# Performance work log

Measured on AMD Instinct MI355X. Metric: run time of the kernel, lower is better.

The kernel has to match this reference:

```python
import jax, jax.numpy as jnp
import numpy as np

B, S, D = 2, 2048, 4096
H, HD = 32, 128  # n_heads, head_dim
P = 30           # prefix_len
ROPE_THETA = 10000.0


def _rope_tables():
    inv = 1.0 / (ROPE_THETA ** (np.arange(0, HD, 2, dtype=np.float64) / HD))
    f = np.outer(np.arange(S, dtype=np.float64), inv)  # [S, HD/2]
    return jnp.asarray(np.cos(f), jnp.float32), jnp.asarray(np.sin(f), jnp.float32)


def setup_inputs() -> dict:
    key = jax.random.key(0)
    ks = jax.random.split(key, 7)
    scale = 0.02
    x = jax.random.normal(ks[0], (B, S, D), jnp.float32)
    freqs_cos, freqs_sin = _rope_tables()
    prefix = jax.random.normal(ks[1], (1, P, D), jnp.float32) * scale
    prefix_gate = jax.random.normal(ks[2], (H,), jnp.float32) * 0.1
    wq = jax.random.normal(ks[3], (D, H * HD), jnp.float32) * scale
    wk = jax.random.normal(ks[4], (D, H * HD), jnp.float32) * scale
    wv = jax.random.normal(ks[5], (D, H * HD), jnp.float32) * scale
    wo = jax.random.normal(ks[6], (H * HD, D), jnp.float32) * scale
    return dict(x=x, freqs_cos=freqs_cos, freqs_sin=freqs_sin, prefix=prefix,
                prefix_gate=prefix_gate, wq=wq, wk=wk, wv=wv, wo=wo, start_pos=0)


def _apply_rope(t, cos, sin):
    # t: [b, s, h, hd]; cos/sin: [s, hd/2] -> broadcast [1, s, 1, hd/2]
    tr = t.reshape(*t.shape[:-1], HD // 2, 2)
    t0, t1 = tr[..., 0], tr[..., 1]
    c = cos[None, :, None, :]
    s = sin[None, :, None, :]
    o0 = t0 * c - t1 * s
    o1 = t0 * s + t1 * c
    return jnp.stack([o0, o1], axis=-1).reshape(t.shape)


def _attend(q, k, v, causal):
    # q: [b, sq, h, d]; k, v: [b, sk, h, d]
    scale = 1.0 / jnp.sqrt(jnp.asarray(HD, q.dtype))
    scores = jnp.einsum('bqhd,bkhd->bhqk', q, k) * scale
    if causal:
        sq, sk = q.shape[1], k.shape[1]
        mask = jnp.tril(jnp.ones((sq, sk), bool))
        scores = jnp.where(mask[None, None], scores, jnp.asarray(-1e30, scores.dtype))
    probs = jax.nn.softmax(scores, axis=-1)
    return jnp.einsum('bhqk,bkhd->bqhd', probs, v)


def reference(x, freqs_cos, freqs_sin, prefix, prefix_gate, wq, wk, wv, wo, start_pos):
    bsz, seqlen, _ = x.shape
    xq = (x @ wq).reshape(bsz, seqlen, H, HD)
    xk = (x @ wk).reshape(bsz, seqlen, H, HD)
    xv = (x @ wv).reshape(bsz, seqlen, H, HD)
    xq = _apply_rope(xq, freqs_cos, freqs_sin)
    xk = _apply_rope(xk, freqs_cos, freqs_sin)
    # n_rep == 1 (MHA), repeat_kv is identity
    out = _attend(xq, xk, xv, causal=True)  # [b, s, h, hd]
    # prefix-tuning branch: no RoPE on prefix k/v, non-causal attention
    pk = jnp.broadcast_to(prefix @ wk, (bsz, P, H * HD)).reshape(bsz, P, H, HD)
    pv = jnp.broadcast_to(prefix @ wv, (bsz, P, H * HD)).reshape(bsz, P, H, HD)
    prefix_delta = _attend(xq, pk, pv, causal=False)
    gate = jnp.tanh(prefix_gate).reshape(1, 1, H, 1)
    out = out + gate * prefix_delta
    out = out.reshape(bsz, seqlen, H * HD)
    return out @ wo
```

## Files before the change

### kernel.cpp

```cpp
#include <hip/hip_runtime.h>
#include <hip/hip_bf16.h>

#define AS1 __attribute__((address_space(1)))
#define AS3 __attribute__((address_space(3)))

typedef __attribute__((ext_vector_type(8))) short bf16x8;
typedef __attribute__((ext_vector_type(4))) float f32x4;

#define B_ 2
#define S_ 2048
#define D_ 4096
#define H_ 32
#define HD_ 128
#define P_ 30

__device__ __forceinline__ short f2b(float f) {
  union { __hip_bfloat16 h; short s; } u;
  u.h = __float2bfloat16(f);
  return u.s;
}
__device__ __forceinline__ float b2f(short s) {
  union { short s; __hip_bfloat16 h; } u;
  u.s = s;
  return __bfloat162float(u.h);
}
__device__ __forceinline__ void gload16(const void* g, void* l) {
  __builtin_amdgcn_global_load_lds((const AS1 void*)g, (AS3 void*)l, 16, 0, 0);
}

__global__ __launch_bounds__(256) void convert_f32_bf16(const float* __restrict__ in,
                                                        short* __restrict__ out) {
  size_t i = ((size_t)blockIdx.x * 256 + threadIdx.x) * 4;
  float4 v = *reinterpret_cast<const float4*>(in + i);
  short4 o;
  o.x = f2b(v.x); o.y = f2b(v.y); o.z = f2b(v.z); o.w = f2b(v.w);
  *reinterpret_cast<short4*>(out + i) = o;
}

__global__ __launch_bounds__(256) void pad_prefix(const float* __restrict__ p,
                                                  short* __restrict__ pb) {
  int i = blockIdx.x * 256 + threadIdx.x;
  int row = i >> 12, col = i & 4095;
  pb[i] = (row < P_) ? f2b(p[row * D_ + col]) : (short)0;
}

__global__ void transpose_convert(const float* __restrict__ W, short* __restrict__ Wt,
                                  int K, int N) {
  __shared__ float t[32][33];
  int bx = blockIdx.x, by = blockIdx.y;
  int tx = threadIdx.x, ty = threadIdx.y;
#pragma unroll
  for (int i = 0; i < 4; ++i) {
    int r = ty * 4 + i;
    t[r][tx] = W[(size_t)(by * 32 + r) * N + bx * 32 + tx];
  }
  __syncthreads();
#pragma unroll
  for (int i = 0; i < 4; ++i) {
    int r = ty * 4 + i;
    Wt[(size_t)(bx * 32 + r) * K + by * 32 + tx] = f2b(t[tx][r]);
  }
}

__global__ __launch_bounds__(256) void rope_kernel(short* __restrict__ q,
                                                   short* __restrict__ k,
                                                   const float* __restrict__ fc,
                                                   const float* __restrict__ fs) {
  short* t = blockIdx.y ? k : q;
  const float qs = blockIdx.y ? 1.0f : 0.08838834764831845f;
  size_t g = ((size_t)blockIdx.x * 256 + threadIdx.x) * 8;
  int d = (int)(g & 127);
  int s = (int)((g >> 12) & 2047);
  bf16x8 v = *reinterpret_cast<bf16x8*>(t + g);
  int i0 = d >> 1;
  float4 c = *reinterpret_cast<const float4*>(fc + (size_t)s * 64 + i0);
  float4 sn = *reinterpret_cast<const float4*>(fs + (size_t)s * 64 + i0);
  float cc[4] = {c.x, c.y, c.z, c.w};
  float ss[4] = {sn.x, sn.y, sn.z, sn.w};
  bf16x8 o;
#pragma unroll
  for (int p = 0; p < 4; ++p) {
    float t0 = b2f(v[2 * p]), t1 = b2f(v[2 * p + 1]);
    o[2 * p] = f2b((t0 * cc[p] - t1 * ss[p]) * qs);
    o[2 * p + 1] = f2b((t0 * ss[p] + t1 * cc[p]) * qs);
  }
  *reinterpret_cast<bf16x8*>(t + g) = o;
}

template <int OM>
__global__ __launch_bounds__(256) void gemm_bt(const short* __restrict__ A,
                                               const short* __restrict__ Bt,
                                               void* __restrict__ Cv,
                                               int M, int N, int K) {
  __shared__ short As[128 * 32];
  __shared__ short Bs[128 * 32];
  const int tid = threadIdx.x;
  const int lane = tid & 63;
  const int wbase = tid & 192;
  const int wr = ((tid >> 7) & 1) * 64;
  const int wc = ((tid >> 6) & 1) * 64;
  const int lr = lane & 15;
  const int lk = (lane >> 4) * 8;
  int lin = blockIdx.y * gridDim.x + blockIdx.x;
  int nwg = gridDim.x * gridDim.y;
  int cpx = nwg >> 3;
  int swz = (lin & 7) * cpx + (lin >> 3);
  const int bm = swz / gridDim.x, bn = swz % gridDim.x;
  f32x4 acc[4][4] = {};
  const short* Ab = A + (size_t)bm * 128 * K;
  const short* Bb = Bt + (size_t)bn * 128 * K;
  for (int kt = 0; kt < K; kt += 32) {
    __syncthreads();
#pragma unroll
    for (int i = 0; i < 2; ++i) {
      int f = i * 256 + tid;
      int row = f >> 2, col = (f & 3) * 8;
      gload16(Ab + (size_t)row * K + kt + col, &As[(i * 256 + wbase) * 8]);
      gload16(Bb + (size_t)row * K + kt + col, &Bs[(i * 256 + wbase) * 8]);
    }
    __syncthreads();
    bf16x8 af[4], bfr[4];
#pragma unroll
    for (int m = 0; m < 4; ++m)
      af[m] = *reinterpret_cast<const bf16x8*>(&As[(wr + m * 16 + lr) * 32 + lk]);
#pragma unroll
    for (int n = 0; n < 4; ++n)
      bfr[n] = *reinterpret_cast<const bf16x8*>(&Bs[(wc + n * 16 + lr) * 32 + lk]);
#pragma unroll
    for (int m = 0; m < 4; ++m)
#pragma unroll
      for (int n = 0; n < 4; ++n)
        acc[m][n] = __builtin_amdgcn_mfma_f32_16x16x32_bf16(af[m], bfr[n], acc[m][n], 0, 0, 0);
  }
  const int row0 = bm * 128 + wr + (lane >> 4) * 4;
  const int col0 = bn * 128 + wc + lr;
  if constexpr (OM == 3) {
    short* C = (short*)Cv;
#pragma unroll
    for (int m = 0; m < 4; ++m)
#pragma unroll
      for (int n = 0; n < 4; ++n) {
        short4 pk;
        pk.x = f2b(acc[m][n][0]); pk.y = f2b(acc[m][n][1]);
        pk.z = f2b(acc[m][n][2]); pk.w = f2b(acc[m][n][3]);
        size_t idx = (size_t)(col0 + n * 16) * M + row0 + m * 16;
        *reinterpret_cast<short4*>(&C[idx]) = pk;
      }
  } else {
#pragma unroll
    for (int m = 0; m < 4; ++m)
#pragma unroll
      for (int n = 0; n < 4; ++n)
#pragma unroll
        for (int j = 0; j < 4; ++j) {
          size_t idx = (size_t)(row0 + m * 16 + j) * N + col0 + n * 16;
          ((short*)Cv)[idx] = f2b(acc[m][n][j]);
        }
  }
}

#define MFMA16(mh)                                                              \
  _Pragma("unroll") for (int mm = 0; mm < 4; ++mm)                              \
    _Pragma("unroll") for (int nn = 0; nn < 4; ++nn)                            \
      acc[(mh)*4 + mm][nn] = __builtin_amdgcn_mfma_f32_16x16x32_bf16(           \
          af[mm], bf[nn], acc[(mh)*4 + mm][nn], 0, 0, 0);

#define PH_SYNC_PRE                                                             \
  __builtin_amdgcn_s_barrier();                                                 \
  asm volatile("s_waitcnt lgkmcnt(0)" ::: "memory");                            \
  __builtin_amdgcn_sched_barrier(0);                                            \
  __builtin_amdgcn_s_setprio(1);

#define PH_SYNC_POST                                                            \
  __builtin_amdgcn_s_setprio(0);                                                \
  __builtin_amdgcn_s_barrier();

template <int OM>
__global__ __launch_bounds__(512, 2) void gemm256(const short* __restrict__ A,
                                                  const short* __restrict__ Bt,
                                                  void* __restrict__ Cv,
                                                  int M, int N, int K) {
  __shared__ short As[2][256 * 64];
  __shared__ short Bs[2][256 * 64];
  const int tid = threadIdx.x;
  const int w = tid >> 6;
  const int lane = tid & 63;
  const int lr = lane & 15, lg = lane >> 4;
  const int wr = (w >> 2) * 128;
  const int wc = (w & 3) * 64;
  int lin = blockIdx.y * gridDim.x + blockIdx.x;
  int nwg = gridDim.x * gridDim.y;
  int cpx = nwg >> 3;
  int swz = (lin & 7) * cpx + (lin >> 3);
  const int bm = swz / gridDim.x, bn = swz % gridDim.x;

  const short* Ab = A + (size_t)bm * 256 * K;
  const short* Bb = Bt + (size_t)bn * 256 * K;
  const int NT = K >> 6;

  f32x4 acc[8][4] = {};

  auto stA = [&](int slot_, int r0, int kt) {
    int row = r0 + (lane >> 3);
    int gsrc = (lane & 7) ^ ((lane >> 3) & 7);
    gload16(Ab + (size_t)row * K + kt + gsrc * 8, &As[slot_][r0 * 64]);
  };
  auto stB = [&](int slot_, int r0, int kt) {
    int row = r0 + (lane >> 3);
    int gsrc = (lane & 7) ^ ((lane >> 3) & 7);
    gload16(Bb + (size_t)row * K + kt + gsrc * 8, &Bs[slot_][r0 * 64]);
  };

  const int q2 = w * 2, q4 = w * 4;
  const int rt0 = (q2 < 8 ? 0 : 64) + q2 * 8;
  const int rt1 = (q2 + 1 < 8 ? 0 : 64) + (q2 + 1) * 8;

  {
#pragma unroll
    for (int i = 0; i < 4; ++i) stB(0, (q4 + i) * 8, 0);
    stA(0, rt0, 0); stA(0, 64 + rt0, 0);
    stA(0, rt1, 0); stA(0, 64 + rt1, 0);
#pragma unroll
    for (int i = 0; i < 4; ++i) stB(1, (q4 + i) * 8, 64);
    stA(1, rt0, 64); stA(1, 64 + rt0, 64);
    stA(1, rt1, 64); stA(1, 64 + rt1, 64);
  }
  asm volatile("s_waitcnt vmcnt(8)" ::: "memory");
  __builtin_amdgcn_s_barrier();

  for (int t = 0; t < NT; ++t) {
    const int slot = t & 1;
    const int ns = slot ^ 1;
    const int kt1 = (t + 1) << 6, kt2 = (t + 2) << 6;
    const bool s6 = (t >= 1) && (t + 1 < NT);
    const bool s2 = (t + 2 < NT);
    bf16x8 bf[4], af[4];

    {
      const int pg = (lg ^ (lr & 7)) * 8;
#pragma unroll
      for (int nn = 0; nn < 4; ++nn)
        bf[nn] = *(const bf16x8*)&Bs[slot][(wc + nn * 16 + lr) * 64 + pg];
#pragma unroll
      for (int mm = 0; mm < 4; ++mm)
        af[mm] = *(const bf16x8*)&As[slot][(wr + mm * 16 + lr) * 64 + pg];
      if (s6) { stB(ns, (q4 + 0) * 8, kt1); stB(ns, (q4 + 1) * 8, kt1);
                stA(ns, 64 + rt0, kt1);     stA(ns, 64 + rt1, kt1); }
      PH_SYNC_PRE
      MFMA16(0)
      PH_SYNC_POST
    }
    {
      const int pg = (lg ^ (lr & 7)) * 8;
#pragma unroll
      for (int mm = 0; mm < 4; ++mm)
        af[mm] = *(const bf16x8*)&As[slot][(wr + 64 + mm * 16 + lr) * 64 + pg];
      if (s6) { stB(ns, (q4 + 2) * 8, kt1); stB(ns, (q4 + 3) * 8, kt1); }
      PH_SYNC_PRE
      MFMA16(1)
      PH_SYNC_POST
    }
    {
      const int pg = ((4 + lg) ^ (lr & 7)) * 8;
#pragma unroll
      for (int nn = 0; nn < 4; ++nn)
        bf[nn] = *(const bf16x8*)&Bs[slot][(wc + nn * 16 + lr) * 64 + pg];
#pragma unroll
      for (int mm = 0; mm < 4; ++mm)
        af[mm] = *(const bf16x8*)&As[slot][(wr + mm * 16 + lr) * 64 + pg];
      PH_SYNC_PRE
      MFMA16(0)
      PH_SYNC_POST
    }
    {
      const int pg = ((4 + lg) ^ (lr & 7)) * 8;
#pragma unroll
      for (int mm = 0; mm < 4; ++mm)
        af[mm] = *(const bf16x8*)&As[slot][(wr + 64 + mm * 16 + lr) * 64 + pg];
      if (s2) { stA(slot, rt0, kt2); stA(slot, rt1, kt2); }
      PH_SYNC_PRE
      MFMA16(1)
      __builtin_amdgcn_s_setprio(0);
      if (s2) asm volatile("s_waitcnt vmcnt(2)" ::: "memory");
      else    asm volatile("s_waitcnt vmcnt(0)" ::: "memory");
      __builtin_amdgcn_s_barrier();
    }
  }

  const int row0 = bm * 256 + wr + lg * 4;
  const int col0 = bn * 256 + wc + lr;
  if constexpr (OM == 2) {
    short* C = (short*)Cv;
#pragma unroll
    for (int mf = 0; mf < 8; ++mf)
#pragma unroll
      for (int n = 0; n < 4; ++n) {
        int r0 = row0 + mf * 16;
        int bb = r0 >> 11, s0 = r0 & 2047;
        short4 pk;
        pk.x = f2b(acc[mf][n][0]); pk.y = f2b(acc[mf][n][1]);
        pk.z = f2b(acc[mf][n][2]); pk.w = f2b(acc[mf][n][3]);
        size_t idx = ((size_t)(bb * 4096 + col0 + n * 16)) * 2048 + s0;
        *reinterpret_cast<short4*>(&C[idx]) = pk;
      }
  } else {
#pragma unroll
    for (int mf = 0; mf < 8; ++mf)
#pragma unroll
      for (int n = 0; n < 4; ++n)
#pragma unroll
        for (int j = 0; j < 4; ++j) {
          size_t idx = (size_t)(row0 + mf * 16 + j) * N + col0 + n * 16;
          if constexpr (OM == 1) ((short*)Cv)[idx] = f2b(acc[mf][n][j]);
          else ((float*)Cv)[idx] = acc[mf][n][j];
        }
  }
}

__global__ __launch_bounds__(1024, 4) void attn_kernel(
    const short* __restrict__ qb, const short* __restrict__ kb, const short* __restrict__ vt,
    const short* __restrict__ pkb, const short* __restrict__ pvt,
    const float* __restrict__ gate, short* __restrict__ ab) {
  __shared__ short Ks[2][64 * 128];
  __shared__ short Vs[2][128 * 64];
  __shared__ short Ps[16][16 * 64];
  const int tid = threadIdx.x;
  const int wave = tid >> 6, lane = tid & 63;
  const int lr = lane & 15, lg = lane >> 4;
  const int lin = blockIdx.x;
  const int qt = 7 - (lin >> 6);
  const int bh = lin & 63;
  const int b = bh >> 5, h = bh & 31;

  bf16x8 aq[4];
  {
    const short* qrow = qb + ((size_t)(b * S_ + qt * 256 + wave * 16 + lr) * H_ + h) * HD_;
#pragma unroll
    for (int kk = 0; kk < 4; ++kk)
      aq[kk] = *reinterpret_cast<const bf16x8*>(qrow + kk * 32 + lg * 8);
  }

  float m = -1e30f, l = 0.f, l2 = 0.f;
  f32x4 o[8] = {}, o2[8] = {};

  const short* kb_bh = kb + ((size_t)b * S_ * H_ + h) * HD_;
  const short* vt_bh = vt + ((size_t)(b * H_ + h)) * HD_ * S_;

  auto stageK = [&](int t, int buf) {
    int row = tid >> 4;
    int col = ((tid & 15) ^ (row & 7)) * 8;
    gload16(kb_bh + (size_t)(t * 64 + row) * (H_ * HD_) + col,
            &Ks[buf][(tid & 960) * 8]);
  };
  auto stagePK = [&](int buf) {
    int row = tid >> 4;
    int col = ((tid & 15) ^ (row & 7)) * 8;
    gload16(pkb + (size_t)row * 4096 + h * HD_ + col, &Ks[buf][(tid & 960) * 8]);
  };
  auto stageV = [&](int t, int buf) {
    int row = tid >> 3;
    int col = ((tid & 7) ^ (row & 7)) * 8;
    gload16(vt_bh + (size_t)row * S_ + t * 64 + col, &Vs[buf][(tid & 1016) * 8]);
  };
  auto stagePV = [&](int buf) {
    int row = tid >> 3;
    int col = ((tid & 7) ^ (row & 7)) * 8;
    gload16(pvt + ((size_t)h * HD_ + row) * 128 + col, &Vs[buf][(tid & 1016) * 8]);
  };

  auto qkt = [&](int buf, f32x4 sc[4]) {
    __builtin_amdgcn_s_setprio(1);
#pragma unroll
    for (int cb = 0; cb < 4; ++cb) {
      int tok = cb * 16 + lr;
#pragma unroll
      for (int kk = 0; kk < 4; ++kk) {
        int addr = tok * 128 + (((kk * 4 + lg) ^ (tok & 7)) * 8);
        bf16x8 bk = *reinterpret_cast<const bf16x8*>(&Ks[buf][addr]);
        sc[cb] = __builtin_amdgcn_mfma_f32_16x16x32_bf16(bk, aq[kk], sc[cb], 0, 0, 0);
      }
    }
    __builtin_amdgcn_s_setprio(0);
  };
  auto pv = [&](int buf, f32x4* acc_) {
#pragma unroll
    for (int kk = 0; kk < 2; ++kk) {
      bf16x8 ap = *reinterpret_cast<const bf16x8*>(
          &Ps[wave][lr * 64 + (((kk * 4 + lg) ^ (lr & 7)) * 8)]);
      __builtin_amdgcn_s_setprio(1);
#pragma unroll
      for (int nb = 0; nb < 8; ++nb) {
        int d = nb * 16 + lr;
        bf16x8 bv = *reinterpret_cast<const bf16x8*>(
            &Vs[buf][d * 64 + (((kk * 4 + lg) ^ (lr & 7)) * 8)]);
        acc_[nb] = __builtin_amdgcn_mfma_f32_16x16x32_bf16(ap, bv, acc_[nb], 0, 0, 0);
      }
      __builtin_amdgcn_s_setprio(0);
    }
  };

  auto process = [&](int t, bool diag) {
    const int buf = t & 1;
    f32x4 sc[4] = {};
    qkt(buf, sc);
    if (diag) {
      const int rowg = qt * 256 + wave * 16 + lr;
#pragma unroll
      for (int cb = 0; cb < 4; ++cb)
#pragma unroll
        for (int j = 0; j < 4; ++j) {
          int colg = t * 64 + cb * 16 + lg * 4 + j;
          if (colg > rowg) sc[cb][j] = -1e30f;
        }
    }
    float mx = sc[0][0];
#pragma unroll
    for (int cb = 0; cb < 4; ++cb)
#pragma unroll
      for (int j = 0; j < 4; ++j) mx = fmaxf(mx, sc[cb][j]);
    mx = fmaxf(mx, __shfl_xor(mx, 16));
    mx = fmaxf(mx, __shfl_xor(mx, 32));
    if (!__all(mx <= m + 8.f)) {
      float mn = fmaxf(m, mx);
      float alpha = __expf(m - mn);
      m = mn;
      l *= alpha;
      f32x4 av;
#pragma unroll
      for (int j = 0; j < 4; ++j) av[j] = __shfl(alpha, lg * 4 + j);
#pragma unroll
      for (int nb = 0; nb < 8; ++nb)
#pragma unroll
        for (int j = 0; j < 4; ++j) o[nb][j] *= av[j];
    }
    float rs = 0.f;
#pragma unroll
    for (int cb = 0; cb < 4; ++cb) {
      short4 pk;
      float p0 = __expf(sc[cb][0] - m);
      float p1 = __expf(sc[cb][1] - m);
      float p2 = __expf(sc[cb][2] - m);
      float p3 = __expf(sc[cb][3] - m);
      rs += (p0 + p1) + (p2 + p3);
      pk.x = f2b(p0); pk.y = f2b(p1); pk.z = f2b(p2); pk.w = f2b(p3);
      int gran = (cb * 2 + (lg >> 1)) ^ (lr & 7);
      *reinterpret_cast<short4*>(&Ps[wave][lr * 64 + gran * 8 + (lg & 1) * 4]) = pk;
    }
    rs += __shfl_xor(rs, 16);
    rs += __shfl_xor(rs, 32);
    l += rs;
    pv(buf, o);
  };

  auto processPrefix = [&]() {
    f32x4 sc[4] = {};
    qkt(0, sc);
#pragma unroll
    for (int cb = 0; cb < 4; ++cb)
#pragma unroll
      for (int j = 0; j < 4; ++j) {
        int coll = cb * 16 + lg * 4 + j;
        if (coll >= P_) sc[cb][j] = -1e30f;
      }
    float mx = sc[0][0];
#pragma unroll
    for (int cb = 0; cb < 4; ++cb)
#pragma unroll
      for (int j = 0; j < 4; ++j) mx = fmaxf(mx, sc[cb][j]);
    mx = fmaxf(mx, __shfl_xor(mx, 16));
    mx = fmaxf(mx, __shfl_xor(mx, 32));
    float rs = 0.f;
#pragma unroll
    for (int cb = 0; cb < 4; ++cb) {
      short4 pk;
      float p0 = __expf(sc[cb][0] - mx);
      float p1 = __expf(sc[cb][1] - mx);
      float p2 = __expf(sc[cb][2] - mx);
      float p3 = __expf(sc[cb][3] - mx);
      rs += (p0 + p1) + (p2 + p3);
      pk.x = f2b(p0); pk.y = f2b(p1); pk.z = f2b(p2); pk.w = f2b(p3);
      int gran = (cb * 2 + (lg >> 1)) ^ (lr & 7);
      *reinterpret_cast<short4*>(&Ps[wave][lr * 64 + gran * 8 + (lg & 1) * 4]) = pk;
    }
    rs += __shfl_xor(rs, 16);
    rs += __shfl_xor(rs, 32);
    l2 = rs;
    pv(0, o2);
  };

  const int nt = 4 * (qt + 1);

  stagePK(0);
  stagePV(0);
  __syncthreads();
  processPrefix();
  __syncthreads();

  stageK(0, 0);
  stageV(0, 0);
  __syncthreads();
  for (int t = 0; t < nt; ++t) {
    if (t + 1 < nt) {
      stageK(t + 1, (t + 1) & 1);
      stageV(t + 1, (t + 1) & 1);
    }
    process(t, t >= 4 * qt);
    __syncthreads();
  }

  {
    float g = tanhf(gate[h]);
    f32x4 lv, lv2;
#pragma unroll
    for (int j = 0; j < 4; ++j) {
      lv[j] = __shfl(l, lg * 4 + j);
      lv2[j] = __shfl(l2, lg * 4 + j);
    }
#pragma unroll
    for (int j = 0; j < 4; ++j) {
      int q = qt * 256 + wave * 16 + lg * 4 + j;
      float inv = 1.f / lv[j];
      float inv2 = g / lv2[j];
      size_t base = ((size_t)(b * S_ + q) * H_ + h) * HD_;
#pragma unroll
      for (int nb = 0; nb < 8; ++nb)
        ab[base + nb * 16 + lr] = f2b(o[nb][j] * inv + o2[nb][j] * inv2);
    }
  }
}

extern "C" void kernel_launch(void* const* d_in, const int* in_sizes, int n_in,
                              void* d_out, int out_size, void* d_ws, size_t ws_size,
                              hipStream_t stream) {
  const float* x = (const float*)d_in[0];
  const float* fc = (const float*)d_in[1];
  const float* fs = (const float*)d_in[2];
  const float* prefix = (const float*)d_in[3];
  const float* gate = (const float*)d_in[4];
  const float* wq = (const float*)d_in[5];
  const float* wk = (const float*)d_in[6];
  const float* wv = (const float*)d_in[7];
  const float* wo = (const float*)d_in[8];
  float* out = (float*)d_out;

  char* ws = (char*)d_ws;
  const size_t SZ = (size_t)4096 * 4096 * 2;
  short* xb = (short*)(ws);
  short* wT = (short*)(ws + SZ);
  short* qbuf = (short*)(ws + 2 * SZ);
  short* kbuf = (short*)(ws + 3 * SZ);
  short* vT = (short*)(ws + 4 * SZ);
  short* pb = (short*)(ws + 5 * SZ);
  short* pkb = (short*)(ws + 5 * SZ + (1 << 20));
  short* pvt = (short*)(ws + 5 * SZ + (2 << 20));
  short* abuf = xb;

  dim3 tcg(128, 128), tcb(32, 8);
  dim3 gg(16, 16), gp(32, 1);

  convert_f32_bf16<<<16384, 256, 0, stream>>>(x, xb);
  pad_prefix<<<2048, 256, 0, stream>>>(prefix, pb);

  transpose_convert<<<tcg, tcb, 0, stream>>>(wq, wT, 4096, 4096);
  gemm256<1><<<gg, 512, 0, stream>>>(xb, wT, qbuf, 4096, 4096, 4096);

  transpose_convert<<<tcg, tcb, 0, stream>>>(wk, wT, 4096, 4096);
  gemm256<1><<<gg, 512, 0, stream>>>(xb, wT, kbuf, 4096, 4096, 4096);
  gemm_bt<1><<<gp, 256, 0, stream>>>(pb, wT, pkb, 128, 4096, 4096);

  transpose_convert<<<tcg, tcb, 0, stream>>>(wv, wT, 4096, 4096);
  gemm256<2><<<gg, 512, 0, stream>>>(xb, wT, vT, 4096, 4096, 4096);
  gemm_bt<3><<<gp, 256, 0, stream>>>(pb, wT, pvt, 128, 4096, 4096);

  rope_kernel<<<dim3(8192, 2), 256, 0, stream>>>(qbuf, kbuf, fc, fs);

  attn_kernel<<<512, 1024, 0, stream>>>(qbuf, kbuf, vT, pkb, pvt, gate, abuf);

  transpose_convert<<<tcg, tcb, 0, stream>>>(wo, wT, 4096, 4096);
  gemm256<0><<<gg, 512, 0, stream>>>(abuf, wT, out, 4096, 4096, 4096);
}
```

Measured before the change: 877.3 us.

## Simplify GEMM main loop to plain double buffering with one barrier per tile

Replaces the four-phase ping-pong schedule, which had per-phase barriers, split prefetches and a two-tile-ahead A prefetch, with a simple double-buffered loop. Each iteration issues the whole next tile's loads up front, runs two k-halves of MFMAs, then waits for all loads and syncs once. This removes intra-tile barriers and lgkm waits. In exchange, prefetch depth drops to one tile and the vmcnt(0) wait at the end of every iteration may expose global load latency.

```diff
diff --git a/kernel.cpp b/kernel.cpp
--- a/kernel.cpp
+++ b/kernel.cpp
@@ -165,16 +165,6 @@
       acc[(mh)*4 + mm][nn] = __builtin_amdgcn_mfma_f32_16x16x32_bf16(           \
           af[mm], bf[nn], acc[(mh)*4 + mm][nn], 0, 0, 0);
 
-#define PH_SYNC_PRE                                                             \
-  __builtin_amdgcn_s_barrier();                                                 \
-  asm volatile("s_waitcnt lgkmcnt(0)" ::: "memory");                            \
-  __builtin_amdgcn_sched_barrier(0);                                            \
-  __builtin_amdgcn_s_setprio(1);
-
-#define PH_SYNC_POST                                                            \
-  __builtin_amdgcn_s_setprio(0);                                                \
-  __builtin_amdgcn_s_barrier();
-
 template <int OM>
 __global__ __launch_bounds__(512, 2) void gemm256(const short* __restrict__ A,
                                                   const short* __restrict__ Bt,
@@ -215,76 +205,45 @@
   const int rt0 = (q2 < 8 ? 0 : 64) + q2 * 8;
   const int rt1 = (q2 + 1 < 8 ? 0 : 64) + (q2 + 1) * 8;
 
-  {
-#pragma unroll
-    for (int i = 0; i < 4; ++i) stB(0, (q4 + i) * 8, 0);
-    stA(0, rt0, 0); stA(0, 64 + rt0, 0);
-    stA(0, rt1, 0); stA(0, 64 + rt1, 0);
-#pragma unroll
-    for (int i = 0; i < 4; ++i) stB(1, (q4 + i) * 8, 64);
-    stA(1, rt0, 64); stA(1, 64 + rt0, 64);
-    stA(1, rt1, 64); stA(1, 64 + rt1, 64);
-  }
-  asm volatile("s_waitcnt vmcnt(8)" ::: "memory");
+  auto stageTile = [&](int slot_, int kt) {
+#pragma unroll
+    for (int i = 0; i < 4; ++i) stB(slot_, (q4 + i) * 8, kt);
+    stA(slot_, rt0, kt); stA(slot_, 64 + rt0, kt);
+    stA(slot_, rt1, kt); stA(slot_, 64 + rt1, kt);
+  };
+
+  stageTile(0, 0);
+  asm volatile("s_waitcnt vmcnt(0)" ::: "memory");
   __builtin_amdgcn_s_barrier();
 
   for (int t = 0; t < NT; ++t) {
     const int slot = t & 1;
     const int ns = slot ^ 1;
-    const int kt1 = (t + 1) << 6, kt2 = (t + 2) << 6;
-    const bool s6 = (t >= 1) && (t + 1 < NT);
-    const bool s2 = (t + 2 < NT);
-    bf16x8 bf[4], af[4];
-
-    {
-      const int pg = (lg ^ (lr & 7)) * 8;
+    if (t + 1 < NT) stageTile(ns, (t + 1) << 6);
+
+#pragma unroll
+    for (int kh = 0; kh < 2; ++kh) {
+      const int pg = ((kh * 4 + lg) ^ (lr & 7)) * 8;
+      bf16x8 bf[4], af[4];
 #pragma unroll
       for (int nn = 0; nn < 4; ++nn)
         bf[nn] = *(const bf16x8*)&Bs[slot][(wc + nn * 16 + lr) * 64 + pg];
 #pragma unroll
       for (int mm = 0; mm < 4; ++mm)
         af[mm] = *(const bf16x8*)&As[slot][(wr + mm * 16 + lr) * 64 + pg];
-      if (s6) { stB(ns, (q4 + 0) * 8, kt1); stB(ns, (q4 + 1) * 8, kt1);
-                stA(ns, 64 + rt0, kt1);     stA(ns, 64 + rt1, kt1); }
-      PH_SYNC_PRE
+      __builtin_amdgcn_s_setprio(1);
       MFMA16(0)
-      PH_SYNC_POST
-    }
-    {
-      const int pg = (lg ^ (lr & 7)) * 8;
+      __builtin_amdgcn_s_setprio(0);
 #pragma unroll
       for (int mm = 0; mm < 4; ++mm)
         af[mm] = *(const bf16x8*)&As[slot][(wr + 64 + mm * 16 + lr) * 64 + pg];
-      if (s6) { stB(ns, (q4 + 2) * 8, kt1); stB(ns, (q4 + 3) * 8, kt1); }
-      PH_SYNC_PRE
-      MFMA16(1)
-      PH_SYNC_POST
-    }
-    {
-      const int pg = ((4 + lg) ^ (lr & 7)) * 8;
-#pragma unroll
-      for (int nn = 0; nn < 4; ++nn)
-        bf[nn] = *(const bf16x8*)&Bs[slot][(wc + nn * 16 + lr) * 64 + pg];
-#pragma unroll
-      for (int mm = 0; mm < 4; ++mm)
-        af[mm] = *(const bf16x8*)&As[slot][(wr + mm * 16 + lr) * 64 + pg];
-      PH_SYNC_PRE
-      MFMA16(0)
-      PH_SYNC_POST
-    }
-    {
-      const int pg = ((4 + lg) ^ (lr & 7)) * 8;
-#pragma unroll
-      for (int mm = 0; mm < 4; ++mm)
-        af[mm] = *(const bf16x8*)&As[slot][(wr + 64 + mm * 16 + lr) * 64 + pg];
-      if (s2) { stA(slot, rt0, kt2); stA(slot, rt1, kt2); }
-      PH_SYNC_PRE
+      __builtin_amdgcn_s_setprio(1);
       MFMA16(1)
       __builtin_amdgcn_s_setprio(0);
-      if (s2) asm volatile("s_waitcnt vmcnt(2)" ::: "memory");
-      else    asm volatile("s_waitcnt vmcnt(0)" ::: "memory");
-      __builtin_amdgcn_s_barrier();
-    }
+    }
+
+    asm volatile("s_waitcnt vmcnt(0)" ::: "memory");
+    __builtin_amdgcn_s_barrier();
   }
 
   const int row0 = bm * 256 + wr + lg * 4;
```

After: 924.8 us. 1.05x slower.
